# Performance work log

Measured on AMD Instinct MI355X. Metric: run time of the kernel, lower is better.

## Reference

```python
import jax, jax.numpy as jnp
import numpy as np

GROUPS = 4
SF = 2   # scale_factor
K = 3    # filter_k

def conv1x1(x, w, b):
    return jnp.einsum('bchw,oc->bohw', x, w) + b[None, :, None, None]

def grid_sample(img, grid):
    # img: (N,C,H,W); grid: (N,Hg,Wg,2) xy in [-1,1]; bilinear, border padding, align_corners=False
    N, C, H, W = img.shape
    ix = jnp.clip(((grid[..., 0] + 1.0) * W - 1.0) * 0.5, 0.0, W - 1.0)
    iy = jnp.clip(((grid[..., 1] + 1.0) * H - 1.0) * 0.5, 0.0, H - 1.0)
    x0 = jnp.floor(ix); y0 = jnp.floor(iy)
    wx = (ix - x0)[..., None]; wy = (iy - y0)[..., None]
    x0i = x0.astype(jnp.int32); y0i = y0.astype(jnp.int32)
    x1i = jnp.minimum(x0i + 1, W - 1); y1i = jnp.minimum(y0i + 1, H - 1)
    bidx = jnp.arange(N)[:, None, None]
    v00 = img[bidx, :, y0i, x0i]; v01 = img[bidx, :, y0i, x1i]
    v10 = img[bidx, :, y1i, x0i]; v11 = img[bidx, :, y1i, x1i]   # (N,Hg,Wg,C)
    out = (v00 * (1 - wx) * (1 - wy) + v01 * wx * (1 - wy)
           + v10 * (1 - wx) * wy + v11 * wx * wy)
    return jnp.transpose(out, (0, 3, 1, 2))

def def_sample(x, off):
    b, c, h, w = x.shape
    g = GROUPS
    off = off.reshape(b * g, SF, SF, 2, h, w).transpose(0, 4, 1, 5, 2, 3)
    hd, wd = SF * h, SF * w
    off = off.reshape(b * g, hd, wd, 2)
    gy, gx = jnp.meshgrid(jnp.arange(hd, dtype=x.dtype) + 0.5,
                          jnp.arange(wd, dtype=x.dtype) + 0.5, indexing='ij')
    base = jnp.stack([gx, gy], axis=-1)[None]
    grid = 2.0 * (base + off) / jnp.array([wd, hd], dtype=x.dtype) - 1.0
    return grid_sample(x.reshape(b * g, c // g, h, w), grid).reshape(b, c, hd, wd)

def dyn_filter(x, compress, kw, kb):
    b, c, h, w = x.shape
    kern = jax.nn.softmax(conv1x1(compress, kw, kb), axis=1)  # (b,K*K,h,w)
    p = K // 2
    xp = jnp.pad(x, ((0, 0), (0, 0), (p, p), (p, p)))
    patches = jnp.stack([xp[:, :, dy:dy + h, dx:dx + w]
                         for dy in range(K) for dx in range(K)], axis=2)  # (b,c,K*K,h,w)
    return jnp.einsum('bkhw,bckhw->bchw', kern, patches)

def trim_op(x, toff):
    b, c, h, w = x.shape
    g = GROUPS
    off = toff.reshape(b, g, 2, h, w).transpose(0, 1, 3, 4, 2)  # (b,g,h,w,2) xy
    gy, gx = jnp.meshgrid(jnp.arange(h, dtype=x.dtype) + 0.5,
                          jnp.arange(w, dtype=x.dtype) + 0.5, indexing='ij')
    base = jnp.stack([gx, gy], axis=-1)[None, None]
    grid = (2.0 * (base + off) / jnp.array([w, h], dtype=x.dtype) - 1.0).reshape(b * g, h, w, 2)
    return grid_sample(x.reshape(b * g, c // g, h, w), grid).reshape(b, c, h, w)

def setup_inputs():
    key = jax.random.key(0)
    ks = jax.random.split(key, 13)
    C = 256
    oc = GROUPS * SF * SF * 2  # 32
    f = jnp.float32
    return {
        "x": jax.random.normal(ks[0], (4, C, 64, 64), f),
        "def_off_w": jax.random.normal(ks[1], (oc, C), f) * 0.001,
        "def_off_b": jnp.zeros((oc,), f),
        "def_ast_w": jax.random.normal(ks[2], (oc, C), f) * 0.01,
        "def_ast_b": jnp.zeros((oc,), f),
        "comp_w": jax.random.normal(ks[3], (64, C), f) * (1.0 / np.sqrt(C).astype(np.float32)),
        "comp_b": jnp.zeros((64,), f),
        "filt_w": jax.random.normal(ks[4], (K * K, 64), f) * 0.001,
        "filt_b": jnp.zeros((K * K,), f),
        "trim_w": jax.random.normal(ks[5], (GROUPS * 2, 64), f) * 0.001,
        "trim_b": jnp.zeros((GROUPS * 2,), f),
        "trim_ast_w": jax.random.normal(ks[6], (GROUPS * 2, 64), f) * 0.01,
        "trim_ast_b": jnp.zeros((GROUPS * 2,), f),
    }

def reference(x, def_off_w, def_off_b, def_ast_w, def_ast_b, comp_w, comp_b,
              filt_w, filt_b, trim_w, trim_b, trim_ast_w, trim_ast_b):
    off = conv1x1(x, def_off_w, def_off_b) * jax.nn.sigmoid(conv1x1(x, def_ast_w, def_ast_b))
    x_up = def_sample(x, off)                              # (b,c,2h,2w)
    comp = conv1x1(x_up, comp_w, comp_b)                   # (b,64,2h,2w)
    x_filt = dyn_filter(x_up, comp, filt_w, filt_b)
    toff = conv1x1(comp, trim_w, trim_b) * jax.nn.sigmoid(conv1x1(comp, trim_ast_w, trim_ast_b))
    return trim_op(x_filt, toff)
```

## Files before the change

kernel.cpp:

```cpp
#include <hip/hip_runtime.h>
#include <hip/hip_bf16.h>
#include <string.h>

typedef __hip_bfloat16 bf16;
typedef __attribute__((ext_vector_type(8))) short short8;
typedef __attribute__((ext_vector_type(4))) short short4v;
typedef __attribute__((ext_vector_type(4))) float f32x4;

__device__ __forceinline__ float b2f(bf16 v) { return __bfloat162float(v); }
__device__ __forceinline__ bf16  f2b(float v) { return __float2bfloat16(v); }
__device__ __forceinline__ float s2f(short s) {
    return __uint_as_float(((unsigned)(unsigned short)s) << 16);
}
__device__ __forceinline__ short f2s(float v) {
    bf16 t = f2b(v); short s; __builtin_memcpy(&s, &t, 2); return s;
}

#define CC 256
#define HWD 16384

__global__ __launch_bounds__(256) void k01_xpose_off(const float* __restrict__ x,
        const float* __restrict__ w_off, const float* __restrict__ b_off,
        const float* __restrict__ w_ast, const float* __restrict__ b_ast,
        bf16* __restrict__ xpm, float* __restrict__ offpm)
{
    __shared__ __align__(16) short tileS[64 * 256];
    const int b = blockIdx.x >> 6;
    const int p0 = (blockIdx.x & 63) << 6;
    const int lane = threadIdx.x & 63;
    const int wave = threadIdx.x >> 6;
    const int n = lane & 15, quad = lane >> 4;

    const int jb = wave << 4;
    const int j = jb + n, oc = j >> 1, kind = j & 1;
    short8 bfrag[8];
    const float* wrow = (kind ? w_ast : w_off) + oc * 256 + quad * 8;
#pragma unroll
    for (int kc = 0; kc < 8; ++kc) {
        float4 lo = *(const float4*)(wrow + kc * 32);
        float4 hi = *(const float4*)(wrow + kc * 32 + 4);
        short8 f;
        f[0] = f2s(lo.x); f[1] = f2s(lo.y); f[2] = f2s(lo.z); f[3] = f2s(lo.w);
        f[4] = f2s(hi.x); f[5] = f2s(hi.y); f[6] = f2s(hi.z); f[7] = f2s(hi.w);
        bfrag[kc] = f;
    }
    float bias = kind ? b_ast[oc] : b_off[oc];

    {
        const float* xb = x + ((size_t)b << 20);
        const int lp = lane;
        const int c0 = wave;
#pragma unroll
        for (int gg = 0; gg < 8; ++gg) {
            int cbase = (c0 << 6) + (gg << 3);
            short8 pk;
#pragma unroll
            for (int jj = 0; jj < 8; ++jj)
                pk[jj] = f2s(xb[((size_t)(cbase + jj) << 12) + p0 + lp]);
            int slot = (cbase >> 3) ^ (lp & 7);
            *(short8*)&tileS[(lp << 8) + (slot << 3)] = pk;
        }
    }
    __syncthreads();

    {
        short* ob = (short*)xpm + ((size_t)((b << 12) + p0) << 8);
#pragma unroll
        for (int rr = 0; rr < 16; ++rr) {
            int r = (wave << 4) + rr;
            short4v v = *(const short4v*)&tileS[(r << 8)
                        + ((((lane >> 1) ^ (r & 7)) << 3) | ((lane & 1) << 2))];
            *(short4v*)(ob + ((size_t)r << 8) + (lane << 2)) = v;
        }
    }

    float* obase = offpm + ((size_t)(b << 12) << 5);
#pragma unroll
    for (int mt = 0; mt < 4; mt += 2) {
        f32x4 acc0 = {0.f, 0.f, 0.f, 0.f};
        f32x4 acc1 = {0.f, 0.f, 0.f, 0.f};
#pragma unroll
        for (int kc = 0; kc < 8; ++kc) {
            int slot = (((kc << 2) + quad) ^ (n & 7)) << 3;
            short8 a0 = *(const short8*)&tileS[((mt * 16 + n) << 8) + slot];
            short8 a1 = *(const short8*)&tileS[((mt * 16 + 16 + n) << 8) + slot];
            acc0 = __builtin_amdgcn_mfma_f32_16x16x32_bf16(a0, bfrag[kc], acc0, 0, 0, 0);
            acc1 = __builtin_amdgcn_mfma_f32_16x16x32_bf16(a1, bfrag[kc], acc1, 0, 0, 0);
        }
#pragma unroll
        for (int r = 0; r < 4; ++r) {
            float v0 = acc0[r] + bias;
            float v1 = acc1[r] + bias;
            float p0v = __shfl_xor(v0, 1, 64);
            float p1v = __shfl_xor(v1, 1, 64);
            if (!(n & 1)) {
                int px = p0 + mt * 16 + quad * 4 + r;
                obase[((size_t)px << 5) + oc] = v0 * (1.f / (1.f + expf(-p0v)));
                obase[((size_t)(px + 16) << 5) + oc] = v1 * (1.f / (1.f + expf(-p1v)));
            }
        }
    }
}

__global__ __launch_bounds__(256) void k23_defsample_comp(
        const bf16* __restrict__ xpm, const float* __restrict__ offpm,
        const float* __restrict__ cw, const float* __restrict__ cb,
        const float* __restrict__ fw_g, const float* __restrict__ fb,
        const float* __restrict__ tw, const float* __restrict__ tb,
        const float* __restrict__ taw, const float* __restrict__ tab,
        bf16* __restrict__ xup, bf16* __restrict__ kern, float* __restrict__ toff)
{
    __shared__ __align__(16) short xupS[64 * 256];
    __shared__ __align__(16) float fwS[64 * 12];
    __shared__ __align__(16) float swS[64 * 16];
    for (int i = threadIdx.x; i < 64 * 12; i += 256) {
        int c = i / 12, k = i % 12;
        fwS[i] = (k < 9) ? fw_g[k * 64 + c] : 0.f;
    }
    for (int i = threadIdx.x; i < 64 * 16; i += 256) {
        int c = i >> 4, jj = i & 15;
        int oc = jj >> 1, kind = jj & 1;
        swS[i] = kind ? taw[oc * 64 + c] : tw[oc * 64 + c];
    }

    const int b = blockIdx.x >> 8;
    const int hw0 = (blockIdx.x & 255) << 6;
    const int lane = threadIdx.x & 63;
    const int wave = threadIdx.x >> 6;
    const int n = lane & 15, quad = lane >> 4;
    const int ocb = wave << 4;

    short8 bfrag[8];
    const float* wrow = cw + (ocb + n) * 256 + quad * 8;
#pragma unroll
    for (int kc = 0; kc < 8; ++kc) {
        float4 lo = *(const float4*)(wrow + kc * 32);
        float4 hi = *(const float4*)(wrow + kc * 32 + 4);
        short8 f;
        f[0] = f2s(lo.x); f[1] = f2s(lo.y); f[2] = f2s(lo.z); f[3] = f2s(lo.w);
        f[4] = f2s(hi.x); f[5] = f2s(hi.y); f[6] = f2s(hi.z); f[7] = f2s(hi.w);
        bfrag[kc] = f;
    }
    float bias = cb[ocb + n];

    {
        const short* xsrc = (const short*)xpm + ((size_t)b << 20);
        const int e = lane << 2;
        const int g = lane >> 4;
#pragma unroll 2
        for (int i = 0; i < 16; ++i) {
            int pp = (wave << 4) + i;
            int hw = hw0 + pp;
            int hy = hw >> 7, wx = hw & 127;
            int h = hy >> 1, w = wx >> 1;
            int och = (g << 3) + ((hy & 1) << 2) + ((wx & 1) << 1);
            const float* orow = offpm + ((size_t)((b << 12) + (h << 6) + w) << 5);
            float ox = orow[och], oy = orow[och + 1];
            float ix = (wx + 0.5f + ox) * 0.5f - 0.5f;
            float iy = (hy + 0.5f + oy) * 0.5f - 0.5f;
            ix = fminf(fmaxf(ix, 0.f), 63.f);
            iy = fminf(fmaxf(iy, 0.f), 63.f);
            float x0f = floorf(ix), y0f = floorf(iy);
            float fx = ix - x0f, fy = iy - y0f;
            int x0 = (int)x0f, y0 = (int)y0f;
            int x1 = min(x0 + 1, 63), y1 = min(y0 + 1, 63);
            float w00 = (1.f - fx) * (1.f - fy), w01 = fx * (1.f - fy);
            float w10 = (1.f - fx) * fy,        w11 = fx * fy;
            short4v v00 = *(const short4v*)(xsrc + (((size_t)(y0 << 6) + x0) << 8) + e);
            short4v v01 = *(const short4v*)(xsrc + (((size_t)(y0 << 6) + x1) << 8) + e);
            short4v v10 = *(const short4v*)(xsrc + (((size_t)(y1 << 6) + x0) << 8) + e);
            short4v v11 = *(const short4v*)(xsrc + (((size_t)(y1 << 6) + x1) << 8) + e);
            short4v pk;
#pragma unroll
            for (int jj = 0; jj < 4; ++jj) {
                float v = w00 * s2f(v00[jj]) + w01 * s2f(v01[jj])
                        + w10 * s2f(v10[jj]) + w11 * s2f(v11[jj]);
                pk[jj] = f2s(v);
            }
            *(short4v*)((short*)xup + (((size_t)((b << 14) + hw)) << 8) + e) = pk;
            *(short4v*)&xupS[(pp << 8)
                    + ((((e >> 3) ^ (pp & 7)) << 3) | (e & 4))] = pk;
        }
    }
    __syncthreads();

    f32x4 accA0 = {0.f,0.f,0.f,0.f}, accA1 = {0.f,0.f,0.f,0.f};
    f32x4 accB0 = {0.f,0.f,0.f,0.f}, accB1 = {0.f,0.f,0.f,0.f};
#pragma unroll
    for (int kc = 0; kc < 8; ++kc) {
        int slot = (((kc << 2) + quad) ^ (n & 7)) << 3;
        short8 a0 = *(const short8*)&xupS[((     n) << 8) + slot];
        short8 a1 = *(const short8*)&xupS[((16 + n) << 8) + slot];
        short8 a2 = *(const short8*)&xupS[((32 + n) << 8) + slot];
        short8 a3 = *(const short8*)&xupS[((48 + n) << 8) + slot];
        accA0 = __builtin_amdgcn_mfma_f32_16x16x32_bf16(a0, bfrag[kc], accA0, 0, 0, 0);
        accA1 = __builtin_amdgcn_mfma_f32_16x16x32_bf16(a1, bfrag[kc], accA1, 0, 0, 0);
        accB0 = __builtin_amdgcn_mfma_f32_16x16x32_bf16(a2, bfrag[kc], accB0, 0, 0, 0);
        accB1 = __builtin_amdgcn_mfma_f32_16x16x32_bf16(a3, bfrag[kc], accB1, 0, 0, 0);
    }
    __syncthreads();

    float (*smc)[65] = (float (*)[65])xupS;
#pragma unroll
    for (int r = 0; r < 4; ++r) {
        smc[     quad * 4 + r][ocb + n] = accA0[r] + bias;
        smc[16 + quad * 4 + r][ocb + n] = accA1[r] + bias;
        smc[32 + quad * 4 + r][ocb + n] = accB0[r] + bias;
        smc[48 + quad * 4 + r][ocb + n] = accB1[r] + bias;
    }
    __syncthreads();

    const int px = threadIdx.x & 63;
    const int q = threadIdx.x >> 6;
    const int hw = hw0 + px;
    if (q == 0) {
        float a[9];
#pragma unroll
        for (int k = 0; k < 9; ++k) a[k] = fb[k];
        for (int c = 0; c < 64; ++c) {
            float v = smc[px][c];
            const float4* wr = reinterpret_cast<const float4*>(&fwS[c * 12]);
            float4 w0 = wr[0], w1 = wr[1];
            float w8 = fwS[c * 12 + 8];
            a[0] += v * w0.x; a[1] += v * w0.y; a[2] += v * w0.z; a[3] += v * w0.w;
            a[4] += v * w1.x; a[5] += v * w1.y; a[6] += v * w1.z; a[7] += v * w1.w;
            a[8] += v * w8;
        }
        float mx = a[0];
#pragma unroll
        for (int k = 1; k < 9; ++k) mx = fmaxf(mx, a[k]);
        float s = 0.f;
#pragma unroll
        for (int k = 0; k < 9; ++k) { a[k] = expf(a[k] - mx); s += a[k]; }
        float inv = 1.f / s;
        short* kr = (short*)kern + ((size_t)((b << 14) + hw) << 4);
        short8 pk;
#pragma unroll
        for (int k = 0; k < 8; ++k) pk[k] = f2s(a[k] * inv);
        *(short8*)kr = pk;
        kr[8] = f2s(a[8] * inv);
    } else {
        const int oc0 = (q == 3) ? 6 : (q - 1) * 3;
        const int noc = (q == 3) ? 2 : 3;
        float o[3], aa[3];
        for (int i = 0; i < noc; ++i) { o[i] = tb[oc0 + i]; aa[i] = tab[oc0 + i]; }
        for (int c = 0; c < 64; ++c) {
            float v = smc[px][c];
            const float* wr = &swS[c << 4];
#pragma unroll 3
            for (int i = 0; i < noc; ++i) {
                o[i]  += v * wr[2 * (oc0 + i)];
                aa[i] += v * wr[2 * (oc0 + i) + 1];
            }
        }
        for (int i = 0; i < noc; ++i)
            toff[((size_t)((b << 3) + oc0 + i) << 14) + hw] =
                o[i] * (1.f / (1.f + expf(-aa[i])));
    }
}

__global__ __launch_bounds__(256) void k4b_apply(const bf16* __restrict__ xup,
        const bf16* __restrict__ kern, bf16* __restrict__ xfilt)
{
    int t = blockIdx.x * 256 + threadIdx.x;
    int chunk = t & 31;
    int hw = (t >> 5) & 16383;
    int b = t >> 19;
    int h = hw >> 7, w = hw & 127;

    const short* kr = (const short*)kern + ((size_t)(b * HWD + hw) << 4);
    short8 k8 = *(const short8*)kr;
    float wk[9];
#pragma unroll
    for (int k = 0; k < 8; ++k) wk[k] = s2f(k8[k]);
    wk[8] = s2f(kr[8]);

    float ymask[3] = { h > 0 ? 1.f : 0.f, 1.f, h < 127 ? 1.f : 0.f };
    float xmask[3] = { w > 0 ? 1.f : 0.f, 1.f, w < 127 ? 1.f : 0.f };
    int hy[3] = { (max(h - 1, 0)) << 7, h << 7, (min(h + 1, 127)) << 7 };
    int wx[3] = { max(w - 1, 0), w, min(w + 1, 127) };

    const short* xb = (const short*)xup + ((size_t)(b * HWD) << 8) + chunk * 8;
    float sum[8];
#pragma unroll
    for (int j = 0; j < 8; ++j) sum[j] = 0.f;
#pragma unroll
    for (int dy = 0; dy < 3; ++dy) {
#pragma unroll
        for (int dx = 0; dx < 3; ++dx) {
            float wgt = wk[dy * 3 + dx] * ymask[dy] * xmask[dx];
            short8 v = *(const short8*)(xb + ((size_t)(hy[dy] + wx[dx]) << 8));
#pragma unroll
            for (int j = 0; j < 8; ++j) sum[j] += wgt * s2f(v[j]);
        }
    }
    short8 pk;
#pragma unroll
    for (int j = 0; j < 8; ++j) pk[j] = f2s(sum[j]);
    *(short8*)((short*)xfilt + ((size_t)(b * HWD + hw) << 8) + chunk * 8) = pk;
}

__global__ __launch_bounds__(256) void k6_trim(const bf16* __restrict__ xfilt,
        const float* __restrict__ toff, float* __restrict__ out)
{
    __shared__ float sm[32][260];
    int b = blockIdx.x >> 9;
    int hw0 = (blockIdx.x & 511) << 5;
    int wave = threadIdx.x >> 6, lane = threadIdx.x & 63;
    int e = lane * 4;
    int g = lane >> 4;
    const short* xb = (const short*)xfilt + ((size_t)(b * HWD) << 8);
    const float* tfx = toff + ((size_t)(b * 8 + 2 * g)     << 14);
    const float* tfy = toff + ((size_t)(b * 8 + 2 * g + 1) << 14);

    for (int i = 0; i < 8; ++i) {
        int pp = wave * 8 + i;
        int hw = hw0 + pp;
        int h = hw >> 7, w = hw & 127;
        float ox = tfx[hw], oy = tfy[hw];
        float ix = fminf(fmaxf(w + ox, 0.f), 127.f);
        float iy = fminf(fmaxf(h + oy, 0.f), 127.f);
        float x0f = floorf(ix), y0f = floorf(iy);
        float fx = ix - x0f, fy = iy - y0f;
        int x0 = (int)x0f, y0 = (int)y0f;
        int x1 = min(x0 + 1, 127), y1 = min(y0 + 1, 127);
        float w00 = (1.f - fx) * (1.f - fy), w01 = fx * (1.f - fy);
        float w10 = (1.f - fx) * fy,        w11 = fx * fy;
        short4v v00 = *(const short4v*)(xb + (((size_t)(y0 << 7) + x0) << 8) + e);
        short4v v01 = *(const short4v*)(xb + (((size_t)(y0 << 7) + x1) << 8) + e);
        short4v v10 = *(const short4v*)(xb + (((size_t)(y1 << 7) + x0) << 8) + e);
        short4v v11 = *(const short4v*)(xb + (((size_t)(y1 << 7) + x1) << 8) + e);
#pragma unroll
        for (int j = 0; j < 4; ++j) {
            sm[pp][e + j] = w00 * s2f(v00[j]) + w01 * s2f(v01[j])
                          + w10 * s2f(v10[j]) + w11 * s2f(v11[j]);
        }
    }
    __syncthreads();
    int lp = threadIdx.x & 31;
    int c0 = (threadIdx.x >> 5) << 5;
    float* ob = out + (((size_t)b << 8) << 14) + hw0 + lp;
#pragma unroll 8
    for (int k = 0; k < 32; ++k) {
        int c = c0 + k;
        ob[(size_t)c << 14] = sm[lp][c];
    }
}

extern "C" void kernel_launch(void* const* d_in, const int* in_sizes, int n_in,
                              void* d_out, int out_size, void* d_ws, size_t ws_size,
                              hipStream_t stream)
{
    const float* x       = (const float*)d_in[0];
    const float* w_off   = (const float*)d_in[1];
    const float* b_off   = (const float*)d_in[2];
    const float* w_ast   = (const float*)d_in[3];
    const float* b_ast   = (const float*)d_in[4];
    const float* comp_w  = (const float*)d_in[5];
    const float* comp_b  = (const float*)d_in[6];
    const float* filt_w  = (const float*)d_in[7];
    const float* filt_b  = (const float*)d_in[8];
    const float* trim_w  = (const float*)d_in[9];
    const float* trim_b  = (const float*)d_in[10];
    const float* trim_aw = (const float*)d_in[11];
    const float* trim_ab = (const float*)d_in[12];
    float* out = (float*)d_out;

    char* ws = (char*)d_ws;
    float* offpm = (float*)(ws);
    bf16*  xup   = (bf16*) (ws + (2ull << 20));
    bf16*  xpm   = (bf16*) (ws + (34ull << 20));
    bf16*  xfilt = (bf16*) (ws + (50ull << 20));
    float* toff  = (float*)(ws + (82ull << 20));
    bf16*  kern  = (bf16*) (ws + (84ull << 20));

    hipLaunchKernelGGL(k01_xpose_off, dim3(256),  dim3(256), 0, stream,
                       x, w_off, b_off, w_ast, b_ast, xpm, offpm);
    hipLaunchKernelGGL(k23_defsample_comp, dim3(1024), dim3(256), 0, stream,
                       xpm, offpm, comp_w, comp_b, filt_w, filt_b,
                       trim_w, trim_b, trim_aw, trim_ab, xup, kern, toff);
    hipLaunchKernelGGL(k4b_apply,   dim3(8192),  dim3(256), 0, stream,
                       xup, kern, xfilt);
    hipLaunchKernelGGL(k6_trim,     dim3(2048),  dim3(256), 0, stream,
                       xfilt, toff, out);
}
```

Baseline: 171.7 us.

## Fuse dynamic filter apply into defsample/comp kernel using 2D tiles with halo

The deformable-sample, compress-conv and softmax kernel now works on 8x8 spatial tiles and recomputes a 10x10 halo of upsampled pixels in shared memory. The 3x3 dynamic filter is then applied directly from LDS, which drops the global xup and kern buffers and the separate apply kernel. The price is about 56% extra bilinear-sampling work for the halo and much more LDS per block, which may lower occupancy. The first kernel also moves to 512 threads, splitting the MFMA row tiles across twice as many waves.

```diff
diff --git a/kernel.cpp b/kernel.cpp
--- a/kernel.cpp
+++ b/kernel.cpp
@@ -16,10 +16,9 @@
     bf16 t = f2b(v); short s; __builtin_memcpy(&s, &t, 2); return s;
 }
 
-#define CC 256
 #define HWD 16384
 
-__global__ __launch_bounds__(256) void k01_xpose_off(const float* __restrict__ x,
+__global__ __launch_bounds__(512) void k01_xpose_off(const float* __restrict__ x,
         const float* __restrict__ w_off, const float* __restrict__ b_off,
         const float* __restrict__ w_ast, const float* __restrict__ b_ast,
         bf16* __restrict__ xpm, float* __restrict__ offpm)
@@ -30,9 +29,10 @@
     const int lane = threadIdx.x & 63;
     const int wave = threadIdx.x >> 6;
     const int n = lane & 15, quad = lane >> 4;
-
-    const int jb = wave << 4;
-    const int j = jb + n, oc = j >> 1, kind = j & 1;
+    const int wq = wave & 3;
+    const int mh = wave >> 2;
+
+    const int j = (wq << 4) + n, oc = j >> 1, kind = j & 1;
     short8 bfrag[8];
     const float* wrow = (kind ? w_ast : w_off) + oc * 256 + quad * 8;
 #pragma unroll
@@ -49,10 +49,9 @@
     {
         const float* xb = x + ((size_t)b << 20);
         const int lp = lane;
-        const int c0 = wave;
-#pragma unroll
-        for (int gg = 0; gg < 8; ++gg) {
-            int cbase = (c0 << 6) + (gg << 3);
+#pragma unroll
+        for (int gg = 0; gg < 4; ++gg) {
+            int cbase = (wave << 5) + (gg << 3);
             short8 pk;
 #pragma unroll
             for (int jj = 0; jj < 8; ++jj)
@@ -66,8 +65,8 @@
     {
         short* ob = (short*)xpm + ((size_t)((b << 12) + p0) << 8);
 #pragma unroll
-        for (int rr = 0; rr < 16; ++rr) {
-            int r = (wave << 4) + rr;
+        for (int rr = 0; rr < 8; ++rr) {
+            int r = (wave << 3) + rr;
             short4v v = *(const short4v*)&tileS[(r << 8)
                         + ((((lane >> 1) ^ (r & 7)) << 3) | ((lane & 1) << 2))];
             *(short4v*)(ob + ((size_t)r << 8) + (lane << 2)) = v;
@@ -75,44 +74,44 @@
     }
 
     float* obase = offpm + ((size_t)(b << 12) << 5);
-#pragma unroll
-    for (int mt = 0; mt < 4; mt += 2) {
-        f32x4 acc0 = {0.f, 0.f, 0.f, 0.f};
-        f32x4 acc1 = {0.f, 0.f, 0.f, 0.f};
-#pragma unroll
-        for (int kc = 0; kc < 8; ++kc) {
-            int slot = (((kc << 2) + quad) ^ (n & 7)) << 3;
-            short8 a0 = *(const short8*)&tileS[((mt * 16 + n) << 8) + slot];
-            short8 a1 = *(const short8*)&tileS[((mt * 16 + 16 + n) << 8) + slot];
-            acc0 = __builtin_amdgcn_mfma_f32_16x16x32_bf16(a0, bfrag[kc], acc0, 0, 0, 0);
-            acc1 = __builtin_amdgcn_mfma_f32_16x16x32_bf16(a1, bfrag[kc], acc1, 0, 0, 0);
-        }
-#pragma unroll
-        for (int r = 0; r < 4; ++r) {
-            float v0 = acc0[r] + bias;
-            float v1 = acc1[r] + bias;
-            float p0v = __shfl_xor(v0, 1, 64);
-            float p1v = __shfl_xor(v1, 1, 64);
-            if (!(n & 1)) {
-                int px = p0 + mt * 16 + quad * 4 + r;
-                obase[((size_t)px << 5) + oc] = v0 * (1.f / (1.f + expf(-p0v)));
-                obase[((size_t)(px + 16) << 5) + oc] = v1 * (1.f / (1.f + expf(-p1v)));
-            }
-        }
-    }
-}
-
-__global__ __launch_bounds__(256) void k23_defsample_comp(
+    f32x4 acc0 = {0.f, 0.f, 0.f, 0.f};
+    f32x4 acc1 = {0.f, 0.f, 0.f, 0.f};
+#pragma unroll
+    for (int kc = 0; kc < 8; ++kc) {
+        int slot = (((kc << 2) + quad) ^ (n & 7)) << 3;
+        short8 a0 = *(const short8*)&tileS[((mh * 32 + n) << 8) + slot];
+        short8 a1 = *(const short8*)&tileS[((mh * 32 + 16 + n) << 8) + slot];
+        acc0 = __builtin_amdgcn_mfma_f32_16x16x32_bf16(a0, bfrag[kc], acc0, 0, 0, 0);
+        acc1 = __builtin_amdgcn_mfma_f32_16x16x32_bf16(a1, bfrag[kc], acc1, 0, 0, 0);
+    }
+#pragma unroll
+    for (int r = 0; r < 4; ++r) {
+        float v0 = acc0[r] + bias;
+        float v1 = acc1[r] + bias;
+        float p0v = __shfl_xor(v0, 1, 64);
+        float p1v = __shfl_xor(v1, 1, 64);
+        if (!(n & 1)) {
+            int px = p0 + mh * 32 + quad * 4 + r;
+            obase[((size_t)px << 5) + oc] = v0 * (1.f / (1.f + expf(-p0v)));
+            obase[((size_t)(px + 16) << 5) + oc] = v1 * (1.f / (1.f + expf(-p1v)));
+        }
+    }
+}
+
+__global__ __launch_bounds__(256, 2) void k234_defsample_comp_filter(
         const bf16* __restrict__ xpm, const float* __restrict__ offpm,
         const float* __restrict__ cw, const float* __restrict__ cb,
         const float* __restrict__ fw_g, const float* __restrict__ fb,
         const float* __restrict__ tw, const float* __restrict__ tb,
         const float* __restrict__ taw, const float* __restrict__ tab,
-        bf16* __restrict__ xup, bf16* __restrict__ kern, float* __restrict__ toff)
+        bf16* __restrict__ xfilt, float* __restrict__ toff)
 {
-    __shared__ __align__(16) short xupS[64 * 256];
+    __shared__ __align__(16) short xupS[100 * 256];
+    __shared__ __align__(16) float smc[64][65];
     __shared__ __align__(16) float fwS[64 * 12];
     __shared__ __align__(16) float swS[64 * 16];
+    __shared__ __align__(16) short kernS[64][18];
+
     for (int i = threadIdx.x; i < 64 * 12; i += 256) {
         int c = i / 12, k = i % 12;
         fwS[i] = (k < 9) ? fw_g[k * 64 + c] : 0.f;
@@ -124,7 +123,8 @@
     }
 
     const int b = blockIdx.x >> 8;
-    const int hw0 = (blockIdx.x & 255) << 6;
+    const int tile = blockIdx.x & 255;
+    const int ty = tile >> 4, tx = tile & 15;
     const int lane = threadIdx.x & 63;
     const int wave = threadIdx.x >> 6;
     const int n = lane & 15, quad = lane >> 4;
@@ -147,11 +147,13 @@
         const short* xsrc = (const short*)xpm + ((size_t)b << 20);
         const int e = lane << 2;
         const int g = lane >> 4;
-#pragma unroll 2
-        for (int i = 0; i < 16; ++i) {
-            int pp = (wave << 4) + i;
-            int hw = hw0 + pp;
-            int hy = hw >> 7, wx = hw & 127;
+#pragma unroll 5
+        for (int i = 0; i < 25; ++i) {
+            int l = wave * 25 + i;
+            int lhy = (l * 205) >> 11;
+            int lwx = l - lhy * 10;
+            int hy = ty * 8 - 1 + lhy;  hy = min(max(hy, 0), 127);
+            int wx = tx * 8 - 1 + lwx;  wx = min(max(wx, 0), 127);
             int h = hy >> 1, w = wx >> 1;
             int och = (g << 3) + ((hy & 1) << 2) + ((wx & 1) << 1);
             const float* orow = offpm + ((size_t)((b << 12) + (h << 6) + w) << 5);
@@ -177,30 +179,30 @@
                         + w10 * s2f(v10[jj]) + w11 * s2f(v11[jj]);
                 pk[jj] = f2s(v);
             }
-            *(short4v*)((short*)xup + (((size_t)((b << 14) + hw)) << 8) + e) = pk;
-            *(short4v*)&xupS[(pp << 8)
-                    + ((((e >> 3) ^ (pp & 7)) << 3) | (e & 4))] = pk;
-        }
-    }
-    __syncthreads();
-
+            *(short4v*)&xupS[(l << 8)
+                    + ((((e >> 3) ^ (l & 7)) << 3) | (e & 4))] = pk;
+        }
+    }
+    __syncthreads();
+
+    const int r0 = (((     n) >> 3) + 1) * 10 + (n & 7) + 1;
+    const int r1 = (((16 + n) >> 3) + 1) * 10 + (n & 7) + 1;
+    const int r2 = (((32 + n) >> 3) + 1) * 10 + (n & 7) + 1;
+    const int r3 = (((48 + n) >> 3) + 1) * 10 + (n & 7) + 1;
     f32x4 accA0 = {0.f,0.f,0.f,0.f}, accA1 = {0.f,0.f,0.f,0.f};
     f32x4 accB0 = {0.f,0.f,0.f,0.f}, accB1 = {0.f,0.f,0.f,0.f};
 #pragma unroll
     for (int kc = 0; kc < 8; ++kc) {
-        int slot = (((kc << 2) + quad) ^ (n & 7)) << 3;
-        short8 a0 = *(const short8*)&xupS[((     n) << 8) + slot];
-        short8 a1 = *(const short8*)&xupS[((16 + n) << 8) + slot];
-        short8 a2 = *(const short8*)&xupS[((32 + n) << 8) + slot];
-        short8 a3 = *(const short8*)&xupS[((48 + n) << 8) + slot];
+        int sp = (kc << 2) + quad;
+        short8 a0 = *(const short8*)&xupS[(r0 << 8) + ((sp ^ (r0 & 7)) << 3)];
+        short8 a1 = *(const short8*)&xupS[(r1 << 8) + ((sp ^ (r1 & 7)) << 3)];
+        short8 a2 = *(const short8*)&xupS[(r2 << 8) + ((sp ^ (r2 & 7)) << 3)];
+        short8 a3 = *(const short8*)&xupS[(r3 << 8) + ((sp ^ (r3 & 7)) << 3)];
         accA0 = __builtin_amdgcn_mfma_f32_16x16x32_bf16(a0, bfrag[kc], accA0, 0, 0, 0);
         accA1 = __builtin_amdgcn_mfma_f32_16x16x32_bf16(a1, bfrag[kc], accA1, 0, 0, 0);
         accB0 = __builtin_amdgcn_mfma_f32_16x16x32_bf16(a2, bfrag[kc], accB0, 0, 0, 0);
         accB1 = __builtin_amdgcn_mfma_f32_16x16x32_bf16(a3, bfrag[kc], accB1, 0, 0, 0);
     }
-    __syncthreads();
-
-    float (*smc)[65] = (float (*)[65])xupS;
 #pragma unroll
     for (int r = 0; r < 4; ++r) {
         smc[     quad * 4 + r][ocb + n] = accA0[r] + bias;
@@ -212,7 +214,6 @@
 
     const int px = threadIdx.x & 63;
     const int q = threadIdx.x >> 6;
-    const int hw = hw0 + px;
     if (q == 0) {
         float a[9];
 #pragma unroll
@@ -233,12 +234,8 @@
 #pragma unroll
         for (int k = 0; k < 9; ++k) { a[k] = expf(a[k] - mx); s += a[k]; }
         float inv = 1.f / s;
-        short* kr = (short*)kern + ((size_t)((b << 14) + hw) << 4);
-        short8 pk;
-#pragma unroll
-        for (int k = 0; k < 8; ++k) pk[k] = f2s(a[k] * inv);
-        *(short8*)kr = pk;
-        kr[8] = f2s(a[8] * inv);
+#pragma unroll
+        for (int k = 0; k < 9; ++k) kernS[px][k] = f2s(a[k] * inv);
     } else {
         const int oc0 = (q == 3) ? 6 : (q - 1) * 3;
         const int noc = (q == 3) ? 2 : 3;
@@ -253,51 +250,51 @@
                 aa[i] += v * wr[2 * (oc0 + i) + 1];
             }
         }
+        int hw = ((ty * 8 + (px >> 3)) << 7) + tx * 8 + (px & 7);
         for (int i = 0; i < noc; ++i)
             toff[((size_t)((b << 3) + oc0 + i) << 14) + hw] =
                 o[i] * (1.f / (1.f + expf(-aa[i])));
     }
-}
-
-__global__ __launch_bounds__(256) void k4b_apply(const bf16* __restrict__ xup,
-        const bf16* __restrict__ kern, bf16* __restrict__ xfilt)
-{
-    int t = blockIdx.x * 256 + threadIdx.x;
-    int chunk = t & 31;
-    int hw = (t >> 5) & 16383;
-    int b = t >> 19;
-    int h = hw >> 7, w = hw & 127;
-
-    const short* kr = (const short*)kern + ((size_t)(b * HWD + hw) << 4);
-    short8 k8 = *(const short8*)kr;
-    float wk[9];
-#pragma unroll
-    for (int k = 0; k < 8; ++k) wk[k] = s2f(k8[k]);
-    wk[8] = s2f(kr[8]);
-
-    float ymask[3] = { h > 0 ? 1.f : 0.f, 1.f, h < 127 ? 1.f : 0.f };
-    float xmask[3] = { w > 0 ? 1.f : 0.f, 1.f, w < 127 ? 1.f : 0.f };
-    int hy[3] = { (max(h - 1, 0)) << 7, h << 7, (min(h + 1, 127)) << 7 };
-    int wx[3] = { max(w - 1, 0), w, min(w + 1, 127) };
-
-    const short* xb = (const short*)xup + ((size_t)(b * HWD) << 8) + chunk * 8;
-    float sum[8];
-#pragma unroll
-    for (int j = 0; j < 8; ++j) sum[j] = 0.f;
-#pragma unroll
-    for (int dy = 0; dy < 3; ++dy) {
-#pragma unroll
-        for (int dx = 0; dx < 3; ++dx) {
-            float wgt = wk[dy * 3 + dx] * ymask[dy] * xmask[dx];
-            short8 v = *(const short8*)(xb + ((size_t)(hy[dy] + wx[dx]) << 8));
-#pragma unroll
-            for (int j = 0; j < 8; ++j) sum[j] += wgt * s2f(v[j]);
-        }
-    }
-    short8 pk;
-#pragma unroll
-    for (int j = 0; j < 8; ++j) pk[j] = f2s(sum[j]);
-    *(short8*)((short*)xfilt + ((size_t)(b * HWD + hw) << 8) + chunk * 8) = pk;
+    __syncthreads();
+
+    {
+        const int chunk = threadIdx.x & 31;
+        const int pxg = threadIdx.x >> 5;
+#pragma unroll
+        for (int it = 0; it < 8; ++it) {
+            int p = (pxg << 3) + it;
+            int ly = p >> 3, lx = p & 7;
+            int gh = ty * 8 + ly, gw = tx * 8 + lx;
+            float wk[9];
+            short8 k8 = *(const short8*)&kernS[p][0];
+#pragma unroll
+            for (int k = 0; k < 8; ++k) wk[k] = s2f(k8[k]);
+            wk[8] = s2f(kernS[p][8]);
+            float ymask[3] = { gh > 0 ? 1.f : 0.f, 1.f, gh < 127 ? 1.f : 0.f };
+            float xmask[3] = { gw > 0 ? 1.f : 0.f, 1.f, gw < 127 ? 1.f : 0.f };
+            float sum[8];
+#pragma unroll
+            for (int jj = 0; jj < 8; ++jj) sum[jj] = 0.f;
+#pragma unroll
+            for (int dy = 0; dy < 3; ++dy) {
+#pragma unroll
+                for (int dx = 0; dx < 3; ++dx) {
+                    float wgt = wk[dy * 3 + dx] * ymask[dy] * xmask[dx];
+                    int r = (ly + dy) * 10 + lx + dx;
+                    short8 v = *(const short8*)&xupS[(r << 8)
+                                + (((chunk ^ (r & 7))) << 3)];
+#pragma unroll
+                    for (int jj = 0; jj < 8; ++jj) sum[jj] += wgt * s2f(v[jj]);
+                }
+            }
+            short8 pk;
+#pragma unroll
+            for (int jj = 0; jj < 8; ++jj) pk[jj] = f2s(sum[jj]);
+            int hw = (gh << 7) + gw;
+            *(short8*)((short*)xfilt + ((size_t)((b << 14) + hw) << 8)
+                       + chunk * 8) = pk;
+        }
+    }
 }
 
 __global__ __launch_bounds__(256) void k6_trim(const bf16* __restrict__ xfilt,
@@ -368,19 +365,15 @@
 
     char* ws = (char*)d_ws;
     float* offpm = (float*)(ws);
-    bf16*  xup   = (bf16*) (ws + (2ull << 20));
-    bf16*  xpm   = (bf16*) (ws + (34ull << 20));
-    bf16*  xfilt = (bf16*) (ws + (50ull << 20));
-    float* toff  = (float*)(ws + (82ull << 20));
-    bf16*  kern  = (bf16*) (ws + (84ull << 20));
-
-    hipLaunchKernelGGL(k01_xpose_off, dim3(256),  dim3(256), 0, stream,
+    bf16*  xpm   = (bf16*) (ws + (2ull << 20));
+    bf16*  xfilt = (bf16*) (ws + (16ull << 20));
+    float* toff  = (float*)(ws + (48ull << 20));
+
+    hipLaunchKernelGGL(k01_xpose_off, dim3(256),  dim3(512), 0, stream,
                        x, w_off, b_off, w_ast, b_ast, xpm, offpm);
-    hipLaunchKernelGGL(k23_defsample_comp, dim3(1024), dim3(256), 0, stream,
+    hipLaunchKernelGGL(k234_defsample_comp_filter, dim3(1024), dim3(256), 0, stream,
                        xpm, offpm, comp_w, comp_b, filt_w, filt_b,
-                       trim_w, trim_b, trim_aw, trim_ab, xup, kern, toff);
-    hipLaunchKernelGGL(k4b_apply,   dim3(8192),  dim3(256), 0, stream,
-                       xup, kern, xfilt);
+                       trim_w, trim_b, trim_aw, trim_ab, xfilt, toff);
     hipLaunchKernelGGL(k6_trim,     dim3(2048),  dim3(256), 0, stream,
                        xfilt, toff, out);
 }
```

Result: slower. 177.1 us (+3.1%).
